# Performance work log

Measured on AMD Instinct MI355X. Metric: run time of the kernel, lower is better.

Reference implementation:

```python
import jax, jax.numpy as jnp
import numpy as np

B, T, V, C, L, H = 2, 1024, 50257, 768, 12, 12
HD = C // H


def setup_inputs() -> dict:
    key = jax.random.key(0)
    ks = jax.random.split(key, 10)
    s = 0.02
    rn = lambda k, shp: (jax.random.normal(k, shp, jnp.float32) * s)
    return dict(
        idx=jax.random.randint(ks[0], (B, T), 0, V),
        wte=rn(ks[1], (V, C)),
        wpe=rn(ks[2], (T, C)),
        ln1_w=jnp.ones((L, C)), ln1_b=jnp.zeros((L, C)),
        attn_w=rn(ks[3], (L, C, 3 * C)), attn_b=jnp.zeros((L, 3 * C)),
        proj_w=rn(ks[4], (L, C, C)), proj_b=jnp.zeros((L, C)),
        ln2_w=jnp.ones((L, C)), ln2_b=jnp.zeros((L, C)),
        fc_w=rn(ks[5], (L, C, 4 * C)), fc_b=jnp.zeros((L, 4 * C)),
        fc2_w=rn(ks[6], (L, 4 * C, C)), fc2_b=jnp.zeros((L, C)),
        lnf_w=jnp.ones((C,)), lnf_b=jnp.zeros((C,)),
        lm_head_w=rn(ks[7], (V, C)),  # torch Linear layout [out, in]
    )


def _layer_norm(x, w, b):
    m = jnp.mean(x, axis=-1, keepdims=True)
    v = jnp.mean(jnp.square(x - m), axis=-1, keepdims=True)
    return (x - m) * jax.lax.rsqrt(v + 1e-5) * w + b


def reference(idx, wte, wpe, ln1_w, ln1_b, attn_w, attn_b, proj_w, proj_b,
              ln2_w, ln2_b, fc_w, fc_b, fc2_w, fc2_b, lnf_w, lnf_b, lm_head_w):
    x = wte[idx] + wpe[jnp.arange(T)]  # [B,T,C]
    mask = jnp.tril(jnp.ones((T, T), bool))

    def block(x, p):
        l1w, l1b, aw, ab, pw, pb, l2w, l2b, fw, fb, f2w, f2b = p
        h = _layer_norm(x, l1w, l1b)
        qkv = h @ aw + ab  # [B,T,3C]
        q, k, v = jnp.split(qkv, 3, axis=-1)
        split_heads = lambda t: t.reshape(B, T, H, HD).transpose(0, 2, 1, 3)
        q, k, v = split_heads(q), split_heads(k), split_heads(v)
        att = jnp.einsum('bhqd,bhkd->bhqk', q, k) * (1.0 / np.sqrt(HD))
        att = jnp.where(mask, att, -jnp.inf)
        att = jax.nn.softmax(att, axis=-1)
        y = jnp.einsum('bhqk,bhkd->bhqd', att, v)
        y = y.transpose(0, 2, 1, 3).reshape(B, T, C)
        x = x + y @ pw + pb
        h2 = _layer_norm(x, l2w, l2b)
        x = x + jax.nn.gelu(h2 @ fw + fb, approximate=True) @ f2w + f2b
        return x, None

    layer_params = (ln1_w, ln1_b, attn_w, attn_b, proj_w, proj_b,
                    ln2_w, ln2_b, fc_w, fc_b, fc2_w, fc2_b)
    x, _ = jax.lax.scan(block, x, layer_params)
    x = _layer_norm(x, lnf_w, lnf_b)
    logits = x @ lm_head_w.T  # [B,T,V]
    return logits
```

## Files before the change

### kernel.cpp

```cpp
#include <hip/hip_runtime.h>
#include <hip/hip_bf16.h>

#define Bsz 2
#define Tsz 1024
#define Vsz 50257
#define Csz 768
#define Lsz 12
#define Hsz 12
#define Msz 2048
#define VPAD 50304

typedef __attribute__((ext_vector_type(8))) short short8;
typedef __attribute__((ext_vector_type(4))) float f32x4;

__device__ __forceinline__ ushort f2bf(float f) {
  union { float f; unsigned u; } v; v.f = f;
  return (ushort)((v.u + 0x7FFFu + ((v.u >> 16) & 1u)) >> 16);
}

__device__ __forceinline__ void load_lds16(const void* g, void* l) {
  __builtin_amdgcn_global_load_lds(
      (const __attribute__((address_space(1))) unsigned int*)g,
      (__attribute__((address_space(3))) unsigned int*)l, 16, 0, 0);
}

__global__ void k_embed(const int* __restrict__ idx, const float* __restrict__ wte,
                        const float* __restrict__ wpe, float* __restrict__ x) {
  int m = blockIdx.x;
  int t = m & (Tsz - 1);
  const float* src = wte + (size_t)idx[m] * Csz;
  const float* pe  = wpe + (size_t)t * Csz;
  float* dst = x + (size_t)m * Csz;
  for (int c = threadIdx.x; c < Csz; c += 256)
    dst[c] = src[c] + pe[c];
}

__global__ void k_ln(const float* __restrict__ x, const float* __restrict__ w,
                     const float* __restrict__ b, ushort* __restrict__ out) {
  int m = blockIdx.x;
  const float* row = x + (size_t)m * Csz;
  int tid = threadIdx.x;
  float v0 = row[tid], v1 = row[tid + 256], v2 = row[tid + 512];
  float s = v0 + v1 + v2;
  float q = v0 * v0 + v1 * v1 + v2 * v2;
  for (int o = 32; o; o >>= 1) {
    s += __shfl_down(s, o, 64);
    q += __shfl_down(q, o, 64);
  }
  __shared__ float red[8];
  __shared__ float mv[2];
  int wid = tid >> 6, lane = tid & 63;
  if (!lane) { red[wid] = s; red[4 + wid] = q; }
  __syncthreads();
  if (!tid) {
    float S = red[0] + red[1] + red[2] + red[3];
    float Q = red[4] + red[5] + red[6] + red[7];
    float mean = S * (1.0f / Csz);
    float var = Q * (1.0f / Csz) - mean * mean;
    mv[0] = mean; mv[1] = rsqrtf(var + 1e-5f);
  }
  __syncthreads();
  float mean = mv[0], rs = mv[1];
  ushort* o = out + (size_t)m * Csz;
  o[tid]       = f2bf((v0 - mean) * rs * w[tid]       + b[tid]);
  o[tid + 256] = f2bf((v1 - mean) * rs * w[tid + 256] + b[tid + 256]);
  o[tid + 512] = f2bf((v2 - mean) * rs * w[tid + 512] + b[tid + 512]);
}

__global__ void k_prep(const float* __restrict__ aw, const float* __restrict__ pw,
                       const float* __restrict__ fw, const float* __restrict__ f2w,
                       ushort* __restrict__ wT, int l0, size_t lstride) {
  int t = blockIdx.x;
  int ly = l0 + blockIdx.y;
  const float* src; int R, Cn; size_t doff;
  if (t < 1728)      { src = aw  + (size_t)ly * Csz * 3 * Csz; R = Csz;     Cn = 3 * Csz; doff = 0; }
  else if (t < 2304) { t -= 1728; src = pw  + (size_t)ly * Csz * Csz;     R = Csz;     Cn = Csz;     doff = (size_t)3 * Csz * Csz; }
  else if (t < 4608) { t -= 2304; src = fw  + (size_t)ly * Csz * 4 * Csz; R = Csz;     Cn = 4 * Csz; doff = (size_t)4 * Csz * Csz; }
  else               { t -= 4608; src = f2w + (size_t)ly * 4 * Csz * Csz; R = 4 * Csz; Cn = Csz;     doff = (size_t)8 * Csz * Csz; }
  ushort* dst = wT + (size_t)blockIdx.y * lstride + doff;

  __shared__ float tb[32][33];
  int ncx = Cn / 32;
  int c0 = (t % ncx) * 32, r0 = (t / ncx) * 32;
  int tx = threadIdx.x & 31, ty = threadIdx.x >> 5;
#pragma unroll
  for (int k = 0; k < 4; k++)
    tb[ty + 8 * k][tx] = src[(size_t)(r0 + ty + 8 * k) * Cn + c0 + tx];
  __syncthreads();
#pragma unroll
  for (int k = 0; k < 4; k++)
    dst[(size_t)(c0 + ty + 8 * k) * R + r0 + tx] = f2bf(tb[tx][ty + 8 * k]);
}

__global__ void k_f32_to_bf16_pad(const float* __restrict__ src, ushort* __restrict__ dst,
                                  int n_src, int n_tot) {
  int stride = gridDim.x * 256 * 4;
  for (int i = (blockIdx.x * 256 + threadIdx.x) * 4; i < n_tot; i += stride) {
    ushort4 o;
    if (i + 3 < n_src) {
      float4 v = *(const float4*)(src + i);
      o.x = f2bf(v.x); o.y = f2bf(v.y); o.z = f2bf(v.z); o.w = f2bf(v.w);
    } else {
      o.x = o.y = o.z = o.w = 0;
    }
    *(ushort4*)(dst + i) = o;
  }
}

template <int BM, int BN, int FM, int FN, int OUT, bool SWZ>
__global__ __launch_bounds__(256) void k_gemm(
    const ushort* __restrict__ A, const ushort* __restrict__ Bt,
    const float* __restrict__ bias, const float* res,
    void* __restrict__ outv, int N, int K, int ntm) {
  constexpr int NCHA = BM / 8, NCH = (BM + BN) / 8, CPW = NCH / 4;
  __shared__ __align__(16) ushort S[2][(BM + BN) * 64];

  int bid = blockIdx.x;
  if (SWZ) {
    int nwg = gridDim.x;
    bid = (bid & 7) * (nwg >> 3) + (bid >> 3);
  }
  int by = bid % ntm, bx = bid / ntm;
  int m0 = by * BM, n0 = bx * BN;

  int tid = threadIdx.x;
  int wid = tid >> 6, lane = tid & 63, lg = lane >> 4, lr = lane & 15;
  int wm = (wid >> 1) * (FM * 16), wn = (wid & 1) * (FN * 16);

  const f32x4 FZ = {0.f, 0.f, 0.f, 0.f};
  f32x4 acc[FM][FN];
#pragma unroll
  for (int i = 0; i < FM; i++)
#pragma unroll
    for (int j = 0; j < FN; j++) acc[i][j] = FZ;

  int srow = lane >> 3;
  int scol = ((lane & 7) ^ srow) * 8;
  int swa = (lr & 7) << 3;

  const ushort* p[CPW];
  int ldso[CPW];
#pragma unroll
  for (int i = 0; i < CPW; i++) {
    int c = wid * CPW + i;
    ldso[i] = c * 512;
    if (c < NCHA) p[i] = A + (size_t)(m0 + c * 8 + srow) * K + scol;
    else          p[i] = Bt + (size_t)(n0 + (c - NCHA) * 8 + srow) * K + scol;
  }

  auto STAGE = [&](int buf) {
#pragma unroll
    for (int i = 0; i < CPW; i++) {
      load_lds16(p[i], &S[buf][ldso[i]]);
      p[i] += 64;
    }
  };
  auto COMPUTE = [&](int buf) {
#pragma unroll
    for (int kk = 0; kk < 2; kk++) {
      int cofs = (kk * 32 + lg * 8) ^ swa;
      short8 a[FM], b[FN];
#pragma unroll
      for (int f = 0; f < FM; f++)
        a[f] = *(const short8*)&S[buf][(wm + f * 16 + lr) * 64 + cofs];
#pragma unroll
      for (int f = 0; f < FN; f++)
        b[f] = *(const short8*)&S[buf][(BM + wn + f * 16 + lr) * 64 + cofs];
#pragma unroll
      for (int fi = 0; fi < FM; fi++)
#pragma unroll
        for (int fj = 0; fj < FN; fj++)
          acc[fi][fj] = __builtin_amdgcn_mfma_f32_16x16x32_bf16(a[fi], b[fj], acc[fi][fj], 0, 0, 0);
    }
  };

  int NT = K >> 6;
  STAGE(0);
  __syncthreads();
  for (int t = 0;;) {
    if (t + 1 < NT) STAGE(1);
    COMPUTE(0);
    if (++t == NT) break;
    __syncthreads();
    if (t + 1 < NT) STAGE(0);
    COMPUTE(1);
    if (++t == NT) break;
    __syncthreads();
  }

#pragma unroll
  for (int fi = 0; fi < FM; fi++)
#pragma unroll
    for (int fj = 0; fj < FN; fj++) {
      int gn = n0 + wn + fj * 16 + lr;
      if (gn < N) {
        float bv = bias ? bias[gn] : 0.f;
#pragma unroll
        for (int i = 0; i < 4; i++) {
          int gm = m0 + wm + fi * 16 + 4 * lg + i;
          size_t o = (size_t)gm * N + gn;
          float v = acc[fi][fj][i] + bv;
          if (OUT == 0) {
            if (res) v += res[o];
            ((float*)outv)[o] = v;
          } else if (OUT == 1) {
            ((ushort*)outv)[o] = f2bf(v);
          } else {
            float u = 0.7978845608f * (v + 0.044715f * v * v * v);
            float t2 = __expf(2.f * u);
            float th = 1.f - 2.f / (t2 + 1.f);
            ((ushort*)outv)[o] = f2bf(0.5f * v * (1.f + th));
          }
        }
      }
    }
}

__global__ __launch_bounds__(256) void k_attn(const ushort* __restrict__ qkv,
                                              ushort* __restrict__ ybf) {
  __shared__ __align__(16) ushort Ks[64 * 72];
  __shared__ __align__(16) ushort Vs[64 * 72];
  __shared__ __align__(16) ushort Ps[4 * 16 * 72];
  int q0 = blockIdx.x * 64;
  int bh = blockIdx.y;
  int b = bh / Hsz, h = bh % Hsz;
  int tid = threadIdx.x, wid = tid >> 6, lane = tid & 63, lg = lane >> 4, lr = lane & 15;
  const ushort* base = qkv + (size_t)b * Tsz * 2304;

  int qt = q0 + wid * 16 + lr;
  const ushort* qp = base + (size_t)qt * 2304 + h * 64;
  short8 aq0 = *(const short8*)(qp + lg * 8);
  short8 aq1 = *(const short8*)(qp + 32 + lg * 8);

  int srow = tid >> 3, soff = (tid & 7) * 8;
  const ushort* kp0 = base + (size_t)srow * 2304 + 768 + h * 64 + soff;
  const ushort* vp0 = kp0 + 768;
  short8 kreg[2], vreg[2];
  auto LOADKV = [&](int k0) {
#pragma unroll
    for (int r = 0; r < 2; r++) {
      kreg[r] = *(const short8*)(kp0 + (size_t)(k0 + r * 32) * 2304);
      vreg[r] = *(const short8*)(vp0 + (size_t)(k0 + r * 32) * 2304);
    }
  };
  auto WRITEKV = [&]() {
#pragma unroll
    for (int r = 0; r < 2; r++) {
      int row = srow + r * 32;
      *(short8*)&Ks[row * 72 + soff] = kreg[r];
#pragma unroll
      for (int j = 0; j < 8; j++) Vs[(soff + j) * 72 + row] = (ushort)vreg[r][j];
    }
  };

  const f32x4 FZ = {0.f, 0.f, 0.f, 0.f};
  f32x4 of[4];
  of[0] = FZ; of[1] = FZ; of[2] = FZ; of[3] = FZ;
  float mrow[4] = {-INFINITY, -INFINITY, -INFINITY, -INFINITY};
  float lrow[4] = {0.f, 0.f, 0.f, 0.f};

  int nkt = q0 / 64 + 1;
  LOADKV(0);
  for (int kt = 0; kt < nkt; kt++) {
    int k0 = kt * 64;
    WRITEKV();
    __syncthreads();
    if (kt + 1 < nkt) LOADKV(k0 + 64);

    f32x4 sf[4];
    sf[0] = FZ; sf[1] = FZ; sf[2] = FZ; sf[3] = FZ;
#pragma unroll
    for (int nf = 0; nf < 4; nf++) {
      short8 b0 = *(const short8*)&Ks[(nf * 16 + lr) * 72 + lg * 8];
      short8 b1 = *(const short8*)&Ks[(nf * 16 + lr) * 72 + 32 + lg * 8];
      sf[nf] = __builtin_amdgcn_mfma_f32_16x16x32_bf16(aq0, b0, sf[nf], 0, 0, 0);
      sf[nf] = __builtin_amdgcn_mfma_f32_16x16x32_bf16(aq1, b1, sf[nf], 0, 0, 0);
    }

    bool last = (kt == nkt - 1);
#pragma unroll
    for (int i = 0; i < 4; i++) {
      int qr = q0 + wid * 16 + 4 * lg + i;
      float s[4];
#pragma unroll
      for (int nf = 0; nf < 4; nf++) {
        s[nf] = sf[nf][i] * 0.125f;
        if (last && k0 + nf * 16 + lr > qr) s[nf] = -INFINITY;
      }
      float rm = fmaxf(fmaxf(s[0], s[1]), fmaxf(s[2], s[3]));
#pragma unroll
      for (int o = 1; o < 16; o <<= 1) rm = fmaxf(rm, __shfl_xor(rm, o, 16));
      float mnew = fmaxf(mrow[i], rm);
      float scale = __expf(mrow[i] - mnew);
      float rs = 0.f;
#pragma unroll
      for (int nf = 0; nf < 4; nf++) {
        float p = __expf(s[nf] - mnew);
        rs += p;
        Ps[(wid * 16 + 4 * lg + i) * 72 + nf * 16 + lr] = f2bf(p);
      }
#pragma unroll
      for (int o = 1; o < 16; o <<= 1) rs += __shfl_xor(rs, o, 16);
      lrow[i] = lrow[i] * scale + rs;
      mrow[i] = mnew;
      of[0][i] *= scale; of[1][i] *= scale; of[2][i] *= scale; of[3][i] *= scale;
    }
    __syncthreads();

    short8 ap0 = *(const short8*)&Ps[(wid * 16 + lr) * 72 + lg * 8];
    short8 ap1 = *(const short8*)&Ps[(wid * 16 + lr) * 72 + 32 + lg * 8];
#pragma unroll
    for (int df = 0; df < 4; df++) {
      short8 bv0 = *(const short8*)&Vs[(df * 16 + lr) * 72 + lg * 8];
      short8 bv1 = *(const short8*)&Vs[(df * 16 + lr) * 72 + 32 + lg * 8];
      of[df] = __builtin_amdgcn_mfma_f32_16x16x32_bf16(ap0, bv0, of[df], 0, 0, 0);
      of[df] = __builtin_amdgcn_mfma_f32_16x16x32_bf16(ap1, bv1, of[df], 0, 0, 0);
    }
    __syncthreads();
  }

  ushort* yp = ybf + (size_t)b * Tsz * Csz;
#pragma unroll
  for (int df = 0; df < 4; df++)
#pragma unroll
    for (int i = 0; i < 4; i++) {
      int qr = q0 + wid * 16 + 4 * lg + i;
      float v = of[df][i] / lrow[i];
      yp[(size_t)qr * Csz + h * 64 + df * 16 + lr] = f2bf(v);
    }
}

extern "C" void kernel_launch(void* const* d_in, const int* in_sizes, int n_in,
                              void* d_out, int out_size, void* d_ws, size_t ws_size,
                              hipStream_t stream) {
  (void)in_sizes; (void)n_in; (void)out_size;
  const int* idx      = (const int*)d_in[0];
  const float* wte    = (const float*)d_in[1];
  const float* wpe    = (const float*)d_in[2];
  const float* ln1_w  = (const float*)d_in[3];
  const float* ln1_b  = (const float*)d_in[4];
  const float* attn_w = (const float*)d_in[5];
  const float* attn_b = (const float*)d_in[6];
  const float* proj_w = (const float*)d_in[7];
  const float* proj_b = (const float*)d_in[8];
  const float* ln2_w  = (const float*)d_in[9];
  const float* ln2_b  = (const float*)d_in[10];
  const float* fc_w   = (const float*)d_in[11];
  const float* fc_b   = (const float*)d_in[12];
  const float* fc2_w  = (const float*)d_in[13];
  const float* fc2_b  = (const float*)d_in[14];
  const float* lnf_w  = (const float*)d_in[15];
  const float* lnf_b  = (const float*)d_in[16];
  const float* lm_w   = (const float*)d_in[17];
  float* out = (float*)d_out;

  char* ws = (char*)d_ws;
  float*  x     = (float*)(ws + 0);
  ushort* qkvbf = (ushort*)(ws + 6291456);
  ushort* abuf  = (ushort*)(ws + 15728640);
  ushort* hbuf  = (ushort*)(ws + 18874368);
  ushort* lmw   = (ushort*)(ws + 31457280);
  ushort* wT    = (ushort*)(ws + 108724224);
  const size_t LSTRIDE = (size_t)12 * Csz * Csz;
  const size_t NEED_FULL = 108724224ull + LSTRIDE * 2 * Lsz;
  bool full = ws_size >= NEED_FULL;

  k_embed<<<Msz, 256, 0, stream>>>(idx, wte, wpe, x);
  k_f32_to_bf16_pad<<<4096, 256, 0, stream>>>(lm_w, lmw, Vsz * Csz, VPAD * Csz);
  if (full)
    k_prep<<<dim3(6912, Lsz), 256, 0, stream>>>(attn_w, proj_w, fc_w, fc2_w, wT, 0, LSTRIDE);

  for (int l = 0; l < Lsz; l++) {
    ushort* wTl = wT + (full ? (size_t)l * LSTRIDE : 0);
    if (!full)
      k_prep<<<dim3(6912, 1), 256, 0, stream>>>(attn_w, proj_w, fc_w, fc2_w, wTl, l, 0);
    const ushort* qkvW = wTl;
    const ushort* projW = wTl + (size_t)3 * Csz * Csz;
    const ushort* fcW   = wTl + (size_t)4 * Csz * Csz;
    const ushort* fc2W  = wTl + (size_t)8 * Csz * Csz;

    k_ln<<<Msz, 256, 0, stream>>>(x, ln1_w + l * Csz, ln1_b + l * Csz, abuf);
    k_gemm<128, 128, 4, 4, 1, false><<<(Msz / 128) * (3 * Csz / 128), 256, 0, stream>>>(
        abuf, qkvW, attn_b + (size_t)l * 3 * Csz, nullptr, qkvbf, 3 * Csz, Csz, Msz / 128);
    k_attn<<<dim3(Tsz / 64, Bsz * Hsz), 256, 0, stream>>>(qkvbf, abuf);
    k_gemm<64, 96, 2, 3, 0, false><<<(Msz / 64) * (Csz / 96), 256, 0, stream>>>(
        abuf, projW, proj_b + (size_t)l * Csz, x, x, Csz, Csz, Msz / 64);
    k_ln<<<Msz, 256, 0, stream>>>(x, ln2_w + l * Csz, ln2_b + l * Csz, abuf);
    k_gemm<128, 128, 4, 4, 2, false><<<(Msz / 128) * (4 * Csz / 128), 256, 0, stream>>>(
        abuf, fcW, fc_b + (size_t)l * 4 * Csz, nullptr, hbuf, 4 * Csz, Csz, Msz / 128);
    k_gemm<64, 96, 2, 3, 0, false><<<(Msz / 64) * (Csz / 96), 256, 0, stream>>>(
        hbuf, fc2W, fc2_b + (size_t)l * Csz, x, x, Csz, 4 * Csz, Msz / 64);
  }

  k_ln<<<Msz, 256, 0, stream>>>(x, lnf_w, lnf_b, abuf);
  int ntm = Msz / 128;
  k_gemm<128, 128, 4, 4, 0, true><<<ntm * (VPAD / 128), 256, 0, stream>>>(
      abuf, lmw, nullptr, nullptr, out, Vsz, Csz, ntm);
}
```

Before: 2.443 ms.

## Add BK template and nontemporal stores; retune QKV and lm_head GEMM tiles

Makes the GEMM K-tile depth a template parameter, with a BK=32 variant that uses its own LDS swizzle and load row mapping. The lm_head GEMM switches to BK=32 and writes its large fp32 logits with nontemporal stores. The QKV GEMM changes to 128x96 tiles, which gives more workgroups. The aims are less LDS per block (so higher occupancy) and less cache pollution from the 400MB logits write, at the cost of more barrier iterations for BK=32.

```diff
diff --git a/kernel.cpp b/kernel.cpp
--- a/kernel.cpp
+++ b/kernel.cpp
@@ -107,13 +107,14 @@
   }
 }
 
-template <int BM, int BN, int FM, int FN, int OUT, bool SWZ>
+template <int BM, int BN, int FM, int FN, int BK, int OUT, bool SWZ, bool NTS>
 __global__ __launch_bounds__(256) void k_gemm(
     const ushort* __restrict__ A, const ushort* __restrict__ Bt,
     const float* __restrict__ bias, const float* res,
     void* __restrict__ outv, int N, int K, int ntm) {
-  constexpr int NCHA = BM / 8, NCH = (BM + BN) / 8, CPW = NCH / 4;
-  __shared__ __align__(16) ushort S[2][(BM + BN) * 64];
+  constexpr int RPC = (BK == 64) ? 8 : 16;
+  constexpr int NCHA = BM / RPC, NCH = (BM + BN) / RPC, CPW = NCH / 4;
+  __shared__ __align__(16) ushort S[2][(BM + BN) * BK];
 
   int bid = blockIdx.x;
   if (SWZ) {
@@ -134,9 +135,9 @@
 #pragma unroll
     for (int j = 0; j < FN; j++) acc[i][j] = FZ;
 
-  int srow = lane >> 3;
-  int scol = ((lane & 7) ^ srow) * 8;
-  int swa = (lr & 7) << 3;
+  int srow, scol;
+  if (BK == 64) { srow = lane >> 3; scol = ((lane & 7) ^ (srow & 7)) * 8; }
+  else          { srow = lane >> 2; scol = ((lane & 3) ^ ((lane >> 3) & 3)) * 8; }
 
   const ushort* p[CPW];
   int ldso[CPW];
@@ -144,28 +145,30 @@
   for (int i = 0; i < CPW; i++) {
     int c = wid * CPW + i;
     ldso[i] = c * 512;
-    if (c < NCHA) p[i] = A + (size_t)(m0 + c * 8 + srow) * K + scol;
-    else          p[i] = Bt + (size_t)(n0 + (c - NCHA) * 8 + srow) * K + scol;
+    if (c < NCHA) p[i] = A + (size_t)(m0 + c * RPC + srow) * K + scol;
+    else          p[i] = Bt + (size_t)(n0 + (c - NCHA) * RPC + srow) * K + scol;
   }
 
   auto STAGE = [&](int buf) {
 #pragma unroll
     for (int i = 0; i < CPW; i++) {
       load_lds16(p[i], &S[buf][ldso[i]]);
-      p[i] += 64;
+      p[i] += BK;
     }
   };
   auto COMPUTE = [&](int buf) {
 #pragma unroll
-    for (int kk = 0; kk < 2; kk++) {
-      int cofs = (kk * 32 + lg * 8) ^ swa;
+    for (int kk = 0; kk < BK / 32; kk++) {
+      int cofs;
+      if (BK == 64) cofs = (kk * 32 + lg * 8) ^ ((lr & 7) << 3);
+      else          cofs = (lg * 8) ^ (((lr >> 1) & 3) << 3);
       short8 a[FM], b[FN];
 #pragma unroll
       for (int f = 0; f < FM; f++)
-        a[f] = *(const short8*)&S[buf][(wm + f * 16 + lr) * 64 + cofs];
+        a[f] = *(const short8*)&S[buf][(wm + f * 16 + lr) * BK + cofs];
 #pragma unroll
       for (int f = 0; f < FN; f++)
-        b[f] = *(const short8*)&S[buf][(BM + wn + f * 16 + lr) * 64 + cofs];
+        b[f] = *(const short8*)&S[buf][(BM + wn + f * 16 + lr) * BK + cofs];
 #pragma unroll
       for (int fi = 0; fi < FM; fi++)
 #pragma unroll
@@ -174,7 +177,7 @@
     }
   };
 
-  int NT = K >> 6;
+  int NT = K / BK;
   STAGE(0);
   __syncthreads();
   for (int t = 0;;) {
@@ -202,7 +205,8 @@
           float v = acc[fi][fj][i] + bv;
           if (OUT == 0) {
             if (res) v += res[o];
-            ((float*)outv)[o] = v;
+            if (NTS) __builtin_nontemporal_store(v, (float*)outv + o);
+            else     ((float*)outv)[o] = v;
           } else if (OUT == 1) {
             ((ushort*)outv)[o] = f2bf(v);
           } else {
@@ -380,20 +384,20 @@
     const ushort* fc2W  = wTl + (size_t)8 * Csz * Csz;
 
     k_ln<<<Msz, 256, 0, stream>>>(x, ln1_w + l * Csz, ln1_b + l * Csz, abuf);
-    k_gemm<128, 128, 4, 4, 1, false><<<(Msz / 128) * (3 * Csz / 128), 256, 0, stream>>>(
+    k_gemm<128, 96, 4, 3, 64, 1, false, false><<<(Msz / 128) * (3 * Csz / 96), 256, 0, stream>>>(
         abuf, qkvW, attn_b + (size_t)l * 3 * Csz, nullptr, qkvbf, 3 * Csz, Csz, Msz / 128);
     k_attn<<<dim3(Tsz / 64, Bsz * Hsz), 256, 0, stream>>>(qkvbf, abuf);
-    k_gemm<64, 96, 2, 3, 0, false><<<(Msz / 64) * (Csz / 96), 256, 0, stream>>>(
+    k_gemm<64, 96, 2, 3, 64, 0, false, false><<<(Msz / 64) * (Csz / 96), 256, 0, stream>>>(
         abuf, projW, proj_b + (size_t)l * Csz, x, x, Csz, Csz, Msz / 64);
     k_ln<<<Msz, 256, 0, stream>>>(x, ln2_w + l * Csz, ln2_b + l * Csz, abuf);
-    k_gemm<128, 128, 4, 4, 2, false><<<(Msz / 128) * (4 * Csz / 128), 256, 0, stream>>>(
+    k_gemm<128, 128, 4, 4, 64, 2, false, false><<<(Msz / 128) * (4 * Csz / 128), 256, 0, stream>>>(
         abuf, fcW, fc_b + (size_t)l * 4 * Csz, nullptr, hbuf, 4 * Csz, Csz, Msz / 128);
-    k_gemm<64, 96, 2, 3, 0, false><<<(Msz / 64) * (Csz / 96), 256, 0, stream>>>(
+    k_gemm<64, 96, 2, 3, 64, 0, false, false><<<(Msz / 64) * (Csz / 96), 256, 0, stream>>>(
         hbuf, fc2W, fc2_b + (size_t)l * Csz, x, x, Csz, 4 * Csz, Msz / 64);
   }
 
   k_ln<<<Msz, 256, 0, stream>>>(x, lnf_w, lnf_b, abuf);
   int ntm = Msz / 128;
-  k_gemm<128, 128, 4, 4, 0, true><<<ntm * (VPAD / 128), 256, 0, stream>>>(
+  k_gemm<128, 128, 4, 4, 32, 0, true, true><<<ntm * (VPAD / 128), 256, 0, stream>>>(
       abuf, lmw, nullptr, nullptr, out, Vsz, Csz, ntm);
 }
```

Measured after the change: 2.566 ms. 5.0% more time.
